# Kernel tuning notes

Hardware: AMD Instinct MI355X
Metric: run time of the kernel (lower is better)

Reference implementation:

```python
import jax, jax.numpy as jnp
import numpy as np

B, C, H, W = 4, 256, 64, 64
C4 = C // 4
EPS = 1e-5  # BatchNorm eps (torch default)


def setup_inputs() -> dict:
    key = jax.random.key(0)
    ks = jax.random.split(key, 24)
    rn = lambda k, s, sc=1.0: jax.random.normal(k, s, jnp.float32) * sc
    un = lambda k, s: jax.random.uniform(k, s, jnp.float32, 0.5, 1.5)
    return {
        "x1": rn(ks[0], (B, C, H, W)),
        "x2": rn(ks[1], (B, C, H, W)),
        "x3": rn(ks[2], (B, C, H, W)),
        # conv_n1: in_c -> in_c//4, 1x1 conv + BN(affine) params
        "w1": rn(ks[3], (C4, C), 0.05), "b1": rn(ks[4], (C4,), 0.05),
        "g1": 1.0 + rn(ks[5], (C4,), 0.05), "be1": rn(ks[6], (C4,), 0.05),
        "m1": rn(ks[7], (C4,), 0.05), "v1": un(ks[8], (C4,)),
        # conv_n2: in_c -> in_c//4
        "w2": rn(ks[9], (C4, C), 0.05), "b2": rn(ks[10], (C4,), 0.05),
        "g2": 1.0 + rn(ks[11], (C4,), 0.05), "be2": rn(ks[12], (C4,), 0.05),
        "m2": rn(ks[13], (C4,), 0.05), "v2": un(ks[14], (C4,)),
        # conv_n3: in_c -> in_c
        "w3": rn(ks[15], (C, C), 0.05), "b3": rn(ks[16], (C,), 0.05),
        "g3": 1.0 + rn(ks[17], (C,), 0.05), "be3": rn(ks[18], (C,), 0.05),
        "m3": rn(ks[19], (C,), 0.05), "v3": un(ks[20], (C,)),
        # gamma residual gate (torch inits to 0; use 0.5 so the attention path matters)
        "gam": jnp.full((1,), 0.5, jnp.float32),
    }


def _cbr(x, w, b, g, be, m, v):
    # 1x1 conv == channel contraction, then inference-mode BN, then ReLU
    y = jnp.einsum("bchw,oc->bohw", x, w) + b[None, :, None, None]
    scale = (g * jax.lax.rsqrt(v + EPS))[None, :, None, None]
    shift = (be - g * m * jax.lax.rsqrt(v + EPS))[None, :, None, None]
    return jax.nn.relu(y * scale + shift)


def reference(x1, x2, x3,
              w1, b1, g1, be1, m1, v1,
              w2, b2, g2, be2, m2, v2,
              w3, b3, g3, be3, m3, v3,
              gam):
    b, c, h, w = x1.shape
    hw = h * w
    q = _cbr(x1, w1, b1, g1, be1, m1, v1).reshape(b, -1, hw).transpose(0, 2, 1)  # (b, hw, c/4)
    k = _cbr(x2, w2, b2, g2, be2, m2, v2).reshape(b, -1, hw)                      # (b, c/4, hw)
    attn = jax.nn.softmax(jnp.einsum("bnc,bcm->bnm", q, k), axis=-1)              # (b, hw, hw)
    val = _cbr(x3, w3, b3, g3, be3, m3, v3).reshape(b, c, hw)                     # (b, c, hw)
    # out[b,c,i] = sum_j val[b,c,j] * attn[b,i,j]   (bmm with attn^T)
    out = jnp.einsum("bcj,bij->bci", val, attn).reshape(b, c, h, w)
    return gam[0] * out + x1
```

## Files before the change

kernel.cpp:

```cpp
#include <hip/hip_runtime.h>
#include <math.h>

#define HW 4096
#define CIN 256
#define BN_EPS 1e-5f
#define LOG2E 1.44269504088896f

typedef __attribute__((ext_vector_type(8))) short short8;
typedef __attribute__((ext_vector_type(4))) float floatx4;
typedef __attribute__((ext_vector_type(4))) unsigned short u16x4;
typedef unsigned short ushort;
typedef unsigned int u32;

__device__ inline ushort f2bf(float f) {
    union { float f; unsigned u; } c; c.f = f;
    unsigned r = c.u + 0x7fff + ((c.u >> 16) & 1);
    return (ushort)(r >> 16);
}
__device__ inline float bf2f(ushort u) {
    union { unsigned u; float f; } c; c.u = ((u32)u) << 16; return c.f;
}

__device__ inline void load_lds16(const ushort* g, ushort* l) {
    __builtin_amdgcn_global_load_lds(
        (const __attribute__((address_space(1))) u32*)g,
        (__attribute__((address_space(3))) u32*)l, 16, 0, 0);
}

__global__ __launch_bounds__(256) void transpose_bf16(
    const float* __restrict__ x1, const float* __restrict__ x2,
    const float* __restrict__ x3, ushort* __restrict__ Xt1,
    ushort* __restrict__ Xt2, ushort* __restrict__ Xt3)
{
    const int z = blockIdx.z;
    const int inp = z >> 2, b = z & 3;
    const float* x = inp == 0 ? x1 : (inp == 1 ? x2 : x3);
    ushort* o = inp == 0 ? Xt1 : (inp == 1 ? Xt2 : Xt3);
    const int c0 = blockIdx.y << 6, p0 = blockIdx.x << 6;
    const int tid = threadIdx.x;

    __shared__ float t[64 * 65];

    const int col = tid & 63, r4 = tid >> 6;
#pragma unroll
    for (int t2 = 0; t2 < 16; t2++) {
        int row = (t2 << 2) + r4;
        t[row * 65 + col] = x[((size_t)(b * CIN + c0 + row) << 12) + p0 + col];
    }
    __syncthreads();
    const int p = tid >> 2, cs = (tid & 3) << 4;
    alignas(16) ushort v[16];
#pragma unroll
    for (int k = 0; k < 16; k++) v[k] = f2bf(t[(cs + k) * 65 + p]);
    size_t base = ((size_t)(b * HW + p0 + p)) * 256 + c0 + cs;
    *(short8*)&o[base]     = *(short8*)&v[0];
    *(short8*)&o[base + 8] = *(short8*)&v[8];
}

__global__ __launch_bounds__(256) void prep_weights(
    const float* __restrict__ w1, const float* __restrict__ b1,
    const float* __restrict__ g1, const float* __restrict__ be1,
    const float* __restrict__ m1, const float* __restrict__ v1,
    const float* __restrict__ w2, const float* __restrict__ b2,
    const float* __restrict__ g2, const float* __restrict__ be2,
    const float* __restrict__ m2, const float* __restrict__ v2,
    const float* __restrict__ w3, const float* __restrict__ b3,
    const float* __restrict__ g3, const float* __restrict__ be3,
    const float* __restrict__ m3, const float* __restrict__ v3,
    ushort* __restrict__ w1c, ushort* __restrict__ w2c, ushort* __restrict__ w3c,
    float* __restrict__ bc)
{
    const int bid = blockIdx.x, tid = threadIdx.x;
    if (bid < 384) {
        int idx = bid * 256 + tid;
        if (idx < 16384) {
            int o = idx >> 8;
            float A = g1[o] * rsqrtf(v1[o] + BN_EPS) * LOG2E;
            w1c[idx] = f2bf(w1[idx] * A);
        } else if (idx < 32768) {
            int i2 = idx - 16384, o = i2 >> 8;
            float A = g2[o] * rsqrtf(v2[o] + BN_EPS);
            w2c[i2] = f2bf(w2[i2] * A);
        } else {
            int i3 = idx - 32768, o = i3 >> 8;
            float A = g3[o] * rsqrtf(v3[o] + BN_EPS);
            w3c[i3] = f2bf(w3[i3] * A);
        }
    } else {
        if (tid < 64) {
            float A = g1[tid] * rsqrtf(v1[tid] + BN_EPS);
            bc[tid] = ((b1[tid] - m1[tid]) * A + be1[tid]) * LOG2E;
        } else if (tid < 128) {
            int o = tid - 64;
            float A = g2[o] * rsqrtf(v2[o] + BN_EPS);
            bc[tid] = (b2[o] - m2[o]) * A + be2[o];
        } else {
#pragma unroll
            for (int t = 0; t < 2; t++) {
                int o = (tid - 128) + t * 128;
                float A = g3[o] * rsqrtf(v3[o] + BN_EPS);
                bc[128 + o] = (b3[o] - m3[o]) * A + be3[o];
            }
        }
    }
}

__global__ __launch_bounds__(256) void gemm_qk(
    const ushort* __restrict__ Xt1, const ushort* __restrict__ Xt2,
    const ushort* __restrict__ w1c, const ushort* __restrict__ w2c,
    const float* __restrict__ bc, ushort* __restrict__ Qw, ushort* __restrict__ Kw)
{
    const int which = blockIdx.z;
    const ushort* X = which ? Xt2 : Xt1;
    const ushort* W = which ? w2c : w1c;
    const float* bias = bc + which * 64;
    ushort* out = which ? Kw : Qw;
    const int b = blockIdx.y;
    const int px0 = blockIdx.x << 6;

    __shared__ alignas(16) ushort Wl[64 * 64];
    __shared__ alignas(16) ushort Xl[64 * 64];

    const int tid = threadIdx.x;
    const int lane = tid & 63;
    const int wv = tid >> 6;
    const int l15 = lane & 15, qd = lane >> 4;
    const int n0w = wv << 4;
    const int sw = l15 & 7;

    floatx4 acc[4];
#pragma unroll
    for (int mt = 0; mt < 4; mt++) acc[mt] = (floatx4){0.f, 0.f, 0.f, 0.f};

    for (int kk = 0; kk < 4; kk++) {
        const int k0 = kk << 6;
        __syncthreads();
#pragma unroll
        for (int t = 0; t < 2; t++) {
            int L = t * 256 + tid;
            int row = L >> 3, c = L & 7;
            load_lds16(W + row * 256 + k0 + ((c ^ (row & 7)) << 3), Wl + L * 8);
            load_lds16(X + ((size_t)(b * HW + px0 + row)) * 256 + k0 + ((c ^ (row & 7)) << 3),
                       Xl + L * 8);
        }
        __syncthreads();
#pragma unroll
        for (int kb = 0; kb < 2; kb++) {
            const int csel = (((kb << 2) + qd) ^ sw) << 3;
            short8 bfr = *(const short8*)&Xl[((n0w + l15) << 6) + csel];
#pragma unroll
            for (int mt = 0; mt < 4; mt++) {
                short8 af = *(const short8*)&Wl[(((mt << 4) + l15) << 6) + csel];
                acc[mt] = __builtin_amdgcn_mfma_f32_16x16x32_bf16(af, bfr, acc[mt], 0, 0, 0);
            }
        }
    }
    const int px = px0 + n0w + l15;
#pragma unroll
    for (int mt = 0; mt < 4; mt++) {
        alignas(8) ushort v4[4];
#pragma unroll
        for (int r = 0; r < 4; r++) {
            int oc = (mt << 4) + (qd << 2) + r;
            v4[r] = f2bf(fmaxf(acc[mt][r] + bias[oc], 0.f));
        }
        *(u16x4*)&out[(((size_t)(b * HW + px)) << 6) + (mt << 4) + (qd << 2)] = *(u16x4*)v4;
    }
}

__global__ __launch_bounds__(256) void gemm_v(
    const ushort* __restrict__ Xt3, const ushort* __restrict__ w3c,
    const float* __restrict__ bc, ushort* __restrict__ Vw)
{
    const int b = blockIdx.y;
    const int px0 = blockIdx.x << 6;
    const int oc0 = blockIdx.z << 7;
    const float* bias = bc + 128;

    __shared__ alignas(16) ushort Xl[64 * 64];
    __shared__ alignas(16) ushort Wl[128 * 64];

    const int tid = threadIdx.x;
    const int lane = tid & 63;
    const int wv = tid >> 6;
    const int l15 = lane & 15, qd = lane >> 4;
    const int wm0 = (wv & 1) << 5, wn0 = (wv >> 1) << 6;
    const int sw = l15 & 7;

    floatx4 acc[2][4];
#pragma unroll
    for (int mt = 0; mt < 2; mt++)
#pragma unroll
        for (int nt = 0; nt < 4; nt++) acc[mt][nt] = (floatx4){0.f, 0.f, 0.f, 0.f};

    for (int kk = 0; kk < 4; kk++) {
        const int k0 = kk << 6;
        __syncthreads();
#pragma unroll
        for (int t = 0; t < 2; t++) {
            int L = t * 256 + tid;
            int row = L >> 3, c = L & 7;
            load_lds16(Xt3 + ((size_t)(b * HW + px0 + row)) * 256 + k0 + ((c ^ (row & 7)) << 3),
                       Xl + L * 8);
        }
#pragma unroll
        for (int t = 0; t < 4; t++) {
            int L = t * 256 + tid;
            int row = L >> 3, c = L & 7;
            load_lds16(w3c + (oc0 + row) * 256 + k0 + ((c ^ (row & 7)) << 3), Wl + L * 8);
        }
        __syncthreads();
#pragma unroll
        for (int kb = 0; kb < 2; kb++) {
            const int csel = (((kb << 2) + qd) ^ sw) << 3;
            short8 af[2], bfr[4];
#pragma unroll
            for (int mt = 0; mt < 2; mt++)
                af[mt] = *(const short8*)&Xl[((wm0 + (mt << 4) + l15) << 6) + csel];
#pragma unroll
            for (int nt = 0; nt < 4; nt++)
                bfr[nt] = *(const short8*)&Wl[((wn0 + (nt << 4) + l15) << 6) + csel];
#pragma unroll
            for (int mt = 0; mt < 2; mt++)
#pragma unroll
                for (int nt = 0; nt < 4; nt++)
                    acc[mt][nt] = __builtin_amdgcn_mfma_f32_16x16x32_bf16(
                        af[mt], bfr[nt], acc[mt][nt], 0, 0, 0);
        }
    }
#pragma unroll
    for (int nt = 0; nt < 4; nt++) {
        int oc = oc0 + wn0 + (nt << 4) + l15;
        float bv = bias[oc];
#pragma unroll
        for (int mt = 0; mt < 2; mt++) {
            alignas(8) ushort v4[4];
#pragma unroll
            for (int r = 0; r < 4; r++)
                v4[r] = f2bf(fmaxf(acc[mt][nt][r] + bv, 0.f));
            size_t base = (((size_t)(b * CIN + oc)) << 12) + px0 + wm0 + (mt << 4) + (qd << 2);
            *(u16x4*)&Vw[base] = *(u16x4*)v4;
        }
    }
}

__global__ __launch_bounds__(512, 4) void flash_mfma(
    const ushort* __restrict__ Q, const ushort* __restrict__ K,
    const ushort* __restrict__ Vtg, ushort* __restrict__ Op0,
    ushort* __restrict__ Op1, float* __restrict__ mlM, float* __restrict__ mlL)
{
    const int tid = threadIdx.x;
    const int lane = tid & 63;
    const int wv = tid >> 6;
    const int it = wv & 3, ch = wv >> 2;
    const int l15 = lane & 15, qd = lane >> 4;
    const int sw = l15 & 7;

    const int bid = blockIdx.x;
    const int s = bid >> 8;
    const int r8 = bid & 255;
    const int b = (r8 & 7) >> 1;
    const int itile = ((r8 >> 3) << 1) | (r8 & 1);
    const int i0 = itile << 6;
    const int jbeg = s << 11;

    __shared__ alignas(16) ushort Kt[64 * 64];
    __shared__ alignas(16) ushort Vt[256 * 64];
    __shared__ alignas(16) ushort Pt[64 * 64];

    const int prow = it * 16 + l15;

    short8 qf[2];
#pragma unroll
    for (int kb = 0; kb < 2; kb++)
        qf[kb] = *(const short8*)(Q + (((size_t)((b << 12) + i0 + prow)) << 6) + kb * 32 + qd * 8);

    const floatx4 zv = {0.f, 0.f, 0.f, 0.f};
    floatx4 acc[8];
#pragma unroll
    for (int ct = 0; ct < 8; ct++) acc[ct] = zv;
    float mrun = -3.0e38f, lrun = 0.f;

    for (int jj = 0; jj < 2048; jj += 64) {
        const int j0 = jbeg + jj;
        __syncthreads();
        {
            int row = tid >> 3, cb = tid & 7;
            load_lds16(K + (((size_t)((b << 12) + j0 + row)) << 6) + ((cb ^ (row & 7)) << 3),
                       Kt + tid * 8);
#pragma unroll
            for (int t2 = 0; t2 < 4; t2++) {
                int idx = tid + (t2 << 9);
                int vr = idx >> 3, vc = idx & 7;
                load_lds16(Vtg + (((size_t)(b * CIN + vr)) << 12) + j0 + ((vc ^ (vr & 7)) << 3),
                           Vt + idx * 8);
            }
        }
        __syncthreads();

        floatx4 st[4];
#pragma unroll
        for (int t = 0; t < 4; t++) st[t] = zv;
#pragma unroll
        for (int kb = 0; kb < 2; kb++) {
            const int csel = (((kb << 2) + qd) ^ sw) << 3;
#pragma unroll
            for (int t = 0; t < 4; t++) {
                short8 kf = *(const short8*)&Kt[(((t << 4) + l15) << 6) + csel];
                st[t] = __builtin_amdgcn_mfma_f32_16x16x32_bf16(kf, qf[kb], st[t], 0, 0, 0);
            }
        }

        float mloc = -3.0e38f;
#pragma unroll
        for (int t = 0; t < 4; t++)
#pragma unroll
            for (int r = 0; r < 4; r++) mloc = fmaxf(mloc, st[t][r]);
        mloc = fmaxf(mloc, __shfl_xor(mloc, 16));
        mloc = fmaxf(mloc, __shfl_xor(mloc, 32));
        float mnew = fmaxf(mrun, mloc);

        float rs = 0.f;
#pragma unroll
        for (int t = 0; t < 4; t++)
#pragma unroll
            for (int r = 0; r < 4; r++) {
                float p = exp2f(st[t][r] - mnew);
                st[t][r] = p;
                rs += p;
            }
        rs += __shfl_xor(rs, 16);
        rs += __shfl_xor(rs, 32);
        float alpha = exp2f(mrun - mnew);
        mrun = mnew;
        lrun = lrun * alpha + rs;

        if (ch == 0) {
#pragma unroll
            for (int t = 0; t < 4; t++) {
                u16x4 pk;
#pragma unroll
                for (int r = 0; r < 4; r++) pk[r] = f2bf(st[t][r]);
                int jb8 = (t << 1) + (qd >> 1);
                *(u16x4*)&Pt[(prow << 6) + (((jb8 ^ sw) << 3) + ((qd & 1) << 2))] = pk;
            }
        }
        __syncthreads();

        if (__any(alpha < 1.0f)) {
#pragma unroll
            for (int ct = 0; ct < 8; ct++) acc[ct] *= alpha;
        }

        short8 pf[2];
#pragma unroll
        for (int kb = 0; kb < 2; kb++)
            pf[kb] = *(const short8*)&Pt[(prow << 6) + ((((kb << 2) + qd) ^ sw) << 3)];
#pragma unroll
        for (int kb = 0; kb < 2; kb++) {
            const int csel = (((kb << 2) + qd) ^ sw) << 3;
#pragma unroll
            for (int ct = 0; ct < 8; ct++) {
                int crow = (ch << 7) + (ct << 4) + l15;
                short8 vf = *(const short8*)&Vt[(crow << 6) + csel];
                acc[ct] = __builtin_amdgcn_mfma_f32_16x16x32_bf16(vf, pf[kb], acc[ct], 0, 0, 0);
            }
        }
    }

    ushort* Op = s ? Op1 : Op0;
    size_t obase = ((size_t)((b << 12) + i0 + prow)) << 8;
#pragma unroll
    for (int ct = 0; ct < 8; ct++) {
        u16x4 pk;
#pragma unroll
        for (int r = 0; r < 4; r++) pk[r] = f2bf(acc[ct][r]);
        *(u16x4*)&Op[obase + (ch << 7) + (ct << 4) + (qd << 2)] = pk;
    }
    if (ch == 0 && qd == 0) {
        int mi = (s << 14) + (b << 12) + i0 + prow;
        mlM[mi] = mrun;
        mlL[mi] = lrun;
    }
}

__global__ __launch_bounds__(256) void merge_out(
    const ushort* __restrict__ Op0, const ushort* __restrict__ Op1,
    const float* __restrict__ mlM, const float* __restrict__ mlL,
    const float* __restrict__ x1, const float* __restrict__ gam,
    float* __restrict__ out)
{
    const int b = blockIdx.z, c0 = blockIdx.y << 6, i0 = blockIdx.x << 6;
    const int tid = threadIdx.x;

    __shared__ float Tl[64][65];
    __shared__ float a0s[64], a1s[64];

    if (tid < 64) {
        int gi = (b << 12) + i0 + tid;
        float m0 = mlM[gi], m1 = mlM[16384 + gi];
        float l0 = mlL[gi], l1 = mlL[16384 + gi];
        float M = fmaxf(m0, m1);
        float w0 = exp2f(m0 - M), w1 = exp2f(m1 - M);
        float gd = gam[0] / (w0 * l0 + w1 * l1);
        a0s[tid] = w0 * gd;
        a1s[tid] = w1 * gd;
    }
    __syncthreads();
#pragma unroll
    for (int k = 0; k < 4; k++) {
        int idx4 = tid + (k << 8);
        int i = idx4 >> 4, c4 = (idx4 & 15) << 2;
        size_t g = ((size_t)((b << 12) + i0 + i)) * 256 + c0 + c4;
        u16x4 p0 = *(const u16x4*)&Op0[g];
        u16x4 p1 = *(const u16x4*)&Op1[g];
        float A0 = a0s[i], A1 = a1s[i];
#pragma unroll
        for (int r = 0; r < 4; r++)
            Tl[c4 + r][i] = A0 * bf2f(p0[r]) + A1 * bf2f(p1[r]);
    }
    __syncthreads();
#pragma unroll
    for (int k = 0; k < 4; k++) {
        int idx4 = tid + (k << 8);
        int c = idx4 >> 4, i4 = (idx4 & 15) << 2;
        size_t g = (((size_t)(b * CIN + c0 + c)) << 12) + i0 + i4;
        float4 xv = *(const float4*)&x1[g];
        float4 o;
        o.x = Tl[c][i4 + 0] + xv.x;
        o.y = Tl[c][i4 + 1] + xv.y;
        o.z = Tl[c][i4 + 2] + xv.z;
        o.w = Tl[c][i4 + 3] + xv.w;
        *(float4*)&out[g] = o;
    }
}

extern "C" void kernel_launch(void* const* d_in, const int* in_sizes, int n_in,
                              void* d_out, int out_size, void* d_ws, size_t ws_size,
                              hipStream_t stream)
{
    const float* x1  = (const float*)d_in[0];
    const float* x2  = (const float*)d_in[1];
    const float* x3  = (const float*)d_in[2];
    const float* w1  = (const float*)d_in[3];
    const float* b1  = (const float*)d_in[4];
    const float* g1  = (const float*)d_in[5];
    const float* be1 = (const float*)d_in[6];
    const float* m1  = (const float*)d_in[7];
    const float* v1  = (const float*)d_in[8];
    const float* w2  = (const float*)d_in[9];
    const float* b2  = (const float*)d_in[10];
    const float* g2  = (const float*)d_in[11];
    const float* be2 = (const float*)d_in[12];
    const float* m2  = (const float*)d_in[13];
    const float* v2  = (const float*)d_in[14];
    const float* w3  = (const float*)d_in[15];
    const float* b3  = (const float*)d_in[16];
    const float* g3  = (const float*)d_in[17];
    const float* be3 = (const float*)d_in[18];
    const float* m3  = (const float*)d_in[19];
    const float* v3  = (const float*)d_in[20];
    const float* gam = (const float*)d_in[21];

    ushort* Xt1 = (ushort*)d_ws;
    ushort* Xt2 = Xt1 + (size_t)4194304;
    ushort* Xt3 = Xt2 + (size_t)4194304;
    ushort* Qw  = Xt3 + (size_t)4194304;
    ushort* Kw  = Qw  + (size_t)1048576;
    ushort* Vw  = Kw  + (size_t)1048576;
    ushort* w1c = Vw  + (size_t)4194304;
    ushort* w2c = w1c + 16384;
    ushort* w3c = w2c + 16384;
    float*  bc  = (float*)(w3c + 65536);

    ushort* Op0 = Xt1;
    ushort* Op1 = Xt2;
    float*  mlM = (float*)Xt3;
    float*  mlL = mlM + 32768;

    transpose_bf16<<<dim3(64, 4, 12), 256, 0, stream>>>(x1, x2, x3, Xt1, Xt2, Xt3);
    prep_weights<<<385, 256, 0, stream>>>(w1, b1, g1, be1, m1, v1,
                                          w2, b2, g2, be2, m2, v2,
                                          w3, b3, g3, be3, m3, v3,
                                          w1c, w2c, w3c, bc);
    gemm_qk<<<dim3(64, 4, 2), 256, 0, stream>>>(Xt1, Xt2, w1c, w2c, bc, Qw, Kw);
    gemm_v <<<dim3(64, 4, 2), 256, 0, stream>>>(Xt3, w3c, bc, Vw);
    flash_mfma<<<512, 512, 0, stream>>>(Qw, Kw, Vw, Op0, Op1, mlM, mlL);
    merge_out<<<dim3(64, 4, 4), 256, 0, stream>>>(Op0, Op1, mlM, mlL, x1, gam, (float*)d_out);
}
```

Baseline: 240.2 us.

## Use Cauchy-Schwarz softmax bound, fuse prep kernels, and retile flash attention

Replaces the online softmax running max with a fixed per-row upper bound, ||q_i||·max_j||k_j||, computed in the QK GEMM epilogue through an atomicMax. This removes the per-tile max reductions and accumulator rescaling. The transpose and weight prep are fused into one launch, as are the Q/K and V GEMMs, and flash attention moves to 1024-thread blocks covering 128 query rows with K/V staging overlapped with compute. The fixed bound risks underflow of exp2 when the bound is loose, and the larger blocks reduce the number of workgroups.

```diff
diff --git a/kernel.cpp b/kernel.cpp
--- a/kernel.cpp
+++ b/kernel.cpp
@@ -27,37 +27,9 @@
         (__attribute__((address_space(3))) u32*)l, 16, 0, 0);
 }
 
-__global__ __launch_bounds__(256) void transpose_bf16(
+__global__ __launch_bounds__(256) void fuse_tp(
     const float* __restrict__ x1, const float* __restrict__ x2,
-    const float* __restrict__ x3, ushort* __restrict__ Xt1,
-    ushort* __restrict__ Xt2, ushort* __restrict__ Xt3)
-{
-    const int z = blockIdx.z;
-    const int inp = z >> 2, b = z & 3;
-    const float* x = inp == 0 ? x1 : (inp == 1 ? x2 : x3);
-    ushort* o = inp == 0 ? Xt1 : (inp == 1 ? Xt2 : Xt3);
-    const int c0 = blockIdx.y << 6, p0 = blockIdx.x << 6;
-    const int tid = threadIdx.x;
-
-    __shared__ float t[64 * 65];
-
-    const int col = tid & 63, r4 = tid >> 6;
-#pragma unroll
-    for (int t2 = 0; t2 < 16; t2++) {
-        int row = (t2 << 2) + r4;
-        t[row * 65 + col] = x[((size_t)(b * CIN + c0 + row) << 12) + p0 + col];
-    }
-    __syncthreads();
-    const int p = tid >> 2, cs = (tid & 3) << 4;
-    alignas(16) ushort v[16];
-#pragma unroll
-    for (int k = 0; k < 16; k++) v[k] = f2bf(t[(cs + k) * 65 + p]);
-    size_t base = ((size_t)(b * HW + p0 + p)) * 256 + c0 + cs;
-    *(short8*)&o[base]     = *(short8*)&v[0];
-    *(short8*)&o[base + 8] = *(short8*)&v[8];
-}
-
-__global__ __launch_bounds__(256) void prep_weights(
+    const float* __restrict__ x3,
     const float* __restrict__ w1, const float* __restrict__ b1,
     const float* __restrict__ g1, const float* __restrict__ be1,
     const float* __restrict__ m1, const float* __restrict__ v1,
@@ -67,320 +39,349 @@
     const float* __restrict__ w3, const float* __restrict__ b3,
     const float* __restrict__ g3, const float* __restrict__ be3,
     const float* __restrict__ m3, const float* __restrict__ v3,
+    ushort* __restrict__ Xt1, ushort* __restrict__ Xt2, ushort* __restrict__ Xt3,
     ushort* __restrict__ w1c, ushort* __restrict__ w2c, ushort* __restrict__ w3c,
-    float* __restrict__ bc)
+    float* __restrict__ bc, unsigned* __restrict__ KmxU)
 {
-    const int bid = blockIdx.x, tid = threadIdx.x;
-    if (bid < 384) {
-        int idx = bid * 256 + tid;
-        if (idx < 16384) {
-            int o = idx >> 8;
-            float A = g1[o] * rsqrtf(v1[o] + BN_EPS) * LOG2E;
-            w1c[idx] = f2bf(w1[idx] * A);
-        } else if (idx < 32768) {
-            int i2 = idx - 16384, o = i2 >> 8;
+    const int z = blockIdx.z;
+    const int tid = threadIdx.x;
+
+    __shared__ float t[64 * 65];
+
+    if (z == 12) {
+        int pid = blockIdx.y * 64 + blockIdx.x;
+        int g0 = pid * 256 + tid;
+        for (int g = g0; g < 98304; g += 65536) {
+            if (g < 16384) {
+                int o = g >> 8;
+                float A = g1[o] * rsqrtf(v1[o] + BN_EPS) * LOG2E;
+                w1c[g] = f2bf(w1[g] * A);
+            } else if (g < 32768) {
+                int i2 = g - 16384, o = i2 >> 8;
+                float A = g2[o] * rsqrtf(v2[o] + BN_EPS);
+                w2c[i2] = f2bf(w2[i2] * A);
+            } else {
+                int i3 = g - 32768, o = i3 >> 8;
+                float A = g3[o] * rsqrtf(v3[o] + BN_EPS);
+                w3c[i3] = f2bf(w3[i3] * A);
+            }
+        }
+        if (g0 < 4) KmxU[g0] = 0u;
+        if (g0 < 64) {
+            float A = g1[g0] * rsqrtf(v1[g0] + BN_EPS);
+            bc[g0] = ((b1[g0] - m1[g0]) * A + be1[g0]) * LOG2E;
+        } else if (g0 < 128) {
+            int o = g0 - 64;
             float A = g2[o] * rsqrtf(v2[o] + BN_EPS);
-            w2c[i2] = f2bf(w2[i2] * A);
-        } else {
-            int i3 = idx - 32768, o = i3 >> 8;
+            bc[g0] = (b2[o] - m2[o]) * A + be2[o];
+        } else if (g0 < 384) {
+            int o = g0 - 128;
             float A = g3[o] * rsqrtf(v3[o] + BN_EPS);
-            w3c[i3] = f2bf(w3[i3] * A);
-        }
-    } else {
-        if (tid < 64) {
-            float A = g1[tid] * rsqrtf(v1[tid] + BN_EPS);
-            bc[tid] = ((b1[tid] - m1[tid]) * A + be1[tid]) * LOG2E;
-        } else if (tid < 128) {
-            int o = tid - 64;
-            float A = g2[o] * rsqrtf(v2[o] + BN_EPS);
-            bc[tid] = (b2[o] - m2[o]) * A + be2[o];
-        } else {
-#pragma unroll
-            for (int t = 0; t < 2; t++) {
-                int o = (tid - 128) + t * 128;
-                float A = g3[o] * rsqrtf(v3[o] + BN_EPS);
-                bc[128 + o] = (b3[o] - m3[o]) * A + be3[o];
-            }
-        }
-    }
-}
-
-__global__ __launch_bounds__(256) void gemm_qk(
+            bc[128 + o] = (b3[o] - m3[o]) * A + be3[o];
+        }
+        return;
+    }
+
+    const int inp = z >> 2, b = z & 3;
+    const float* x = inp == 0 ? x1 : (inp == 1 ? x2 : x3);
+    ushort* o = inp == 0 ? Xt1 : (inp == 1 ? Xt2 : Xt3);
+    const int c0 = blockIdx.y << 6, p0 = blockIdx.x << 6;
+
+    const int col = tid & 63, r4 = tid >> 6;
+#pragma unroll
+    for (int t2 = 0; t2 < 16; t2++) {
+        int row = (t2 << 2) + r4;
+        t[row * 65 + col] = x[((size_t)(b * CIN + c0 + row) << 12) + p0 + col];
+    }
+    __syncthreads();
+    const int p = tid >> 2, cs = (tid & 3) << 4;
+    alignas(16) ushort v[16];
+#pragma unroll
+    for (int k = 0; k < 16; k++) v[k] = f2bf(t[(cs + k) * 65 + p]);
+    size_t base = ((size_t)(b * HW + p0 + p)) * 256 + c0 + cs;
+    *(short8*)&o[base]     = *(short8*)&v[0];
+    *(short8*)&o[base + 8] = *(short8*)&v[8];
+}
+
+__global__ __launch_bounds__(256) void gemm_qkv(
     const ushort* __restrict__ Xt1, const ushort* __restrict__ Xt2,
+    const ushort* __restrict__ Xt3,
     const ushort* __restrict__ w1c, const ushort* __restrict__ w2c,
-    const float* __restrict__ bc, ushort* __restrict__ Qw, ushort* __restrict__ Kw)
+    const ushort* __restrict__ w3c, const float* __restrict__ bc,
+    ushort* __restrict__ Qw, ushort* __restrict__ Kw, ushort* __restrict__ Vw,
+    float* __restrict__ Qn, unsigned* __restrict__ KmxU)
 {
-    const int which = blockIdx.z;
-    const ushort* X = which ? Xt2 : Xt1;
-    const ushort* W = which ? w2c : w1c;
-    const float* bias = bc + which * 64;
-    ushort* out = which ? Kw : Qw;
+    const int z = blockIdx.z;
     const int b = blockIdx.y;
     const int px0 = blockIdx.x << 6;
-
-    __shared__ alignas(16) ushort Wl[64 * 64];
-    __shared__ alignas(16) ushort Xl[64 * 64];
-
-    const int tid = threadIdx.x;
-    const int lane = tid & 63;
-    const int wv = tid >> 6;
+    const int tid = threadIdx.x, lane = tid & 63, wv = tid >> 6;
     const int l15 = lane & 15, qd = lane >> 4;
-    const int n0w = wv << 4;
     const int sw = l15 & 7;
-
-    floatx4 acc[4];
-#pragma unroll
-    for (int mt = 0; mt < 4; mt++) acc[mt] = (floatx4){0.f, 0.f, 0.f, 0.f};
-
-    for (int kk = 0; kk < 4; kk++) {
-        const int k0 = kk << 6;
-        __syncthreads();
-#pragma unroll
-        for (int t = 0; t < 2; t++) {
-            int L = t * 256 + tid;
-            int row = L >> 3, c = L & 7;
-            load_lds16(W + row * 256 + k0 + ((c ^ (row & 7)) << 3), Wl + L * 8);
-            load_lds16(X + ((size_t)(b * HW + px0 + row)) * 256 + k0 + ((c ^ (row & 7)) << 3),
-                       Xl + L * 8);
-        }
-        __syncthreads();
-#pragma unroll
-        for (int kb = 0; kb < 2; kb++) {
-            const int csel = (((kb << 2) + qd) ^ sw) << 3;
-            short8 bfr = *(const short8*)&Xl[((n0w + l15) << 6) + csel];
-#pragma unroll
-            for (int mt = 0; mt < 4; mt++) {
-                short8 af = *(const short8*)&Wl[(((mt << 4) + l15) << 6) + csel];
-                acc[mt] = __builtin_amdgcn_mfma_f32_16x16x32_bf16(af, bfr, acc[mt], 0, 0, 0);
-            }
-        }
-    }
-    const int px = px0 + n0w + l15;
-#pragma unroll
-    for (int mt = 0; mt < 4; mt++) {
-        alignas(8) ushort v4[4];
-#pragma unroll
-        for (int r = 0; r < 4; r++) {
-            int oc = (mt << 4) + (qd << 2) + r;
-            v4[r] = f2bf(fmaxf(acc[mt][r] + bias[oc], 0.f));
-        }
-        *(u16x4*)&out[(((size_t)(b * HW + px)) << 6) + (mt << 4) + (qd << 2)] = *(u16x4*)v4;
-    }
-}
-
-__global__ __launch_bounds__(256) void gemm_v(
-    const ushort* __restrict__ Xt3, const ushort* __restrict__ w3c,
-    const float* __restrict__ bc, ushort* __restrict__ Vw)
-{
-    const int b = blockIdx.y;
-    const int px0 = blockIdx.x << 6;
-    const int oc0 = blockIdx.z << 7;
-    const float* bias = bc + 128;
 
     __shared__ alignas(16) ushort Xl[64 * 64];
     __shared__ alignas(16) ushort Wl[128 * 64];
 
-    const int tid = threadIdx.x;
-    const int lane = tid & 63;
-    const int wv = tid >> 6;
-    const int l15 = lane & 15, qd = lane >> 4;
-    const int wm0 = (wv & 1) << 5, wn0 = (wv >> 1) << 6;
-    const int sw = l15 & 7;
-
-    floatx4 acc[2][4];
-#pragma unroll
-    for (int mt = 0; mt < 2; mt++)
-#pragma unroll
-        for (int nt = 0; nt < 4; nt++) acc[mt][nt] = (floatx4){0.f, 0.f, 0.f, 0.f};
-
-    for (int kk = 0; kk < 4; kk++) {
-        const int k0 = kk << 6;
-        __syncthreads();
-#pragma unroll
-        for (int t = 0; t < 2; t++) {
-            int L = t * 256 + tid;
-            int row = L >> 3, c = L & 7;
-            load_lds16(Xt3 + ((size_t)(b * HW + px0 + row)) * 256 + k0 + ((c ^ (row & 7)) << 3),
-                       Xl + L * 8);
-        }
-#pragma unroll
-        for (int t = 0; t < 4; t++) {
-            int L = t * 256 + tid;
-            int row = L >> 3, c = L & 7;
-            load_lds16(w3c + (oc0 + row) * 256 + k0 + ((c ^ (row & 7)) << 3), Wl + L * 8);
-        }
-        __syncthreads();
-#pragma unroll
-        for (int kb = 0; kb < 2; kb++) {
-            const int csel = (((kb << 2) + qd) ^ sw) << 3;
-            short8 af[2], bfr[4];
-#pragma unroll
-            for (int mt = 0; mt < 2; mt++)
-                af[mt] = *(const short8*)&Xl[((wm0 + (mt << 4) + l15) << 6) + csel];
-#pragma unroll
-            for (int nt = 0; nt < 4; nt++)
-                bfr[nt] = *(const short8*)&Wl[((wn0 + (nt << 4) + l15) << 6) + csel];
-#pragma unroll
-            for (int mt = 0; mt < 2; mt++)
+    if (z < 2) {
+        const ushort* X = z ? Xt2 : Xt1;
+        const ushort* W = z ? w2c : w1c;
+        const float* bias = bc + (z << 6);
+        ushort* out = z ? Kw : Qw;
+        const int n0w = wv << 4;
+
+        floatx4 acc[4];
+#pragma unroll
+        for (int mt = 0; mt < 4; mt++) acc[mt] = (floatx4){0.f, 0.f, 0.f, 0.f};
+
+        for (int kk = 0; kk < 4; kk++) {
+            const int k0 = kk << 6;
+            __syncthreads();
+#pragma unroll
+            for (int t = 0; t < 2; t++) {
+                int L = t * 256 + tid;
+                int row = L >> 3, c8 = L & 7;
+                load_lds16(W + row * 256 + k0 + ((c8 ^ (row & 7)) << 3), Wl + L * 8);
+                load_lds16(X + ((size_t)((b << 12) + px0 + row)) * 256 + k0 +
+                               ((c8 ^ (row & 7)) << 3), Xl + L * 8);
+            }
+            __syncthreads();
+#pragma unroll
+            for (int kb = 0; kb < 2; kb++) {
+                const int csel = (((kb << 2) + qd) ^ sw) << 3;
+                short8 bfr = *(const short8*)&Xl[((n0w + l15) << 6) + csel];
+#pragma unroll
+                for (int mt = 0; mt < 4; mt++) {
+                    short8 af = *(const short8*)&Wl[(((mt << 4) + l15) << 6) + csel];
+                    acc[mt] = __builtin_amdgcn_mfma_f32_16x16x32_bf16(af, bfr, acc[mt], 0, 0, 0);
+                }
+            }
+        }
+        const int px = px0 + n0w + l15;
+        float s2 = 0.f;
+#pragma unroll
+        for (int mt = 0; mt < 4; mt++) {
+            alignas(8) ushort v4[4];
+#pragma unroll
+            for (int r = 0; r < 4; r++) {
+                int oc = (mt << 4) + (qd << 2) + r;
+                float y = fmaxf(acc[mt][r] + bias[oc], 0.f);
+                s2 += y * y;
+                v4[r] = f2bf(y);
+            }
+            *(u16x4*)&out[(((size_t)((b << 12) + px)) << 6) + (mt << 4) + (qd << 2)] =
+                *(u16x4*)v4;
+        }
+        s2 += __shfl_xor(s2, 16);
+        s2 += __shfl_xor(s2, 32);
+        if (z == 0) {
+            if (qd == 0) Qn[(b << 12) + px] = sqrtf(s2);
+        } else {
+#pragma unroll
+            for (int off = 1; off < 16; off <<= 1) s2 = fmaxf(s2, __shfl_xor(s2, off));
+            if (lane == 0) atomicMax(KmxU + b, __float_as_uint(sqrtf(s2)));
+        }
+    } else {
+        const int oc0 = (z - 2) << 7;
+        const float* bias = bc + 128;
+        const int wm0 = (wv & 1) << 5, wn0 = (wv >> 1) << 6;
+
+        floatx4 acc[2][4];
+#pragma unroll
+        for (int mt = 0; mt < 2; mt++)
+#pragma unroll
+            for (int nt = 0; nt < 4; nt++) acc[mt][nt] = (floatx4){0.f, 0.f, 0.f, 0.f};
+
+        for (int kk = 0; kk < 4; kk++) {
+            const int k0 = kk << 6;
+            __syncthreads();
+#pragma unroll
+            for (int t = 0; t < 2; t++) {
+                int L = t * 256 + tid;
+                int row = L >> 3, c8 = L & 7;
+                load_lds16(Xt3 + ((size_t)((b << 12) + px0 + row)) * 256 + k0 +
+                               ((c8 ^ (row & 7)) << 3), Xl + L * 8);
+            }
+#pragma unroll
+            for (int t = 0; t < 4; t++) {
+                int L = t * 256 + tid;
+                int row = L >> 3, c8 = L & 7;
+                load_lds16(w3c + (oc0 + row) * 256 + k0 + ((c8 ^ (row & 7)) << 3), Wl + L * 8);
+            }
+            __syncthreads();
+#pragma unroll
+            for (int kb = 0; kb < 2; kb++) {
+                const int csel = (((kb << 2) + qd) ^ sw) << 3;
+                short8 af[2], bfr[4];
+#pragma unroll
+                for (int mt = 0; mt < 2; mt++)
+                    af[mt] = *(const short8*)&Xl[((wm0 + (mt << 4) + l15) << 6) + csel];
 #pragma unroll
                 for (int nt = 0; nt < 4; nt++)
-                    acc[mt][nt] = __builtin_amdgcn_mfma_f32_16x16x32_bf16(
-                        af[mt], bfr[nt], acc[mt][nt], 0, 0, 0);
-        }
-    }
-#pragma unroll
-    for (int nt = 0; nt < 4; nt++) {
-        int oc = oc0 + wn0 + (nt << 4) + l15;
-        float bv = bias[oc];
-#pragma unroll
-        for (int mt = 0; mt < 2; mt++) {
-            alignas(8) ushort v4[4];
-#pragma unroll
-            for (int r = 0; r < 4; r++)
-                v4[r] = f2bf(fmaxf(acc[mt][nt][r] + bv, 0.f));
-            size_t base = (((size_t)(b * CIN + oc)) << 12) + px0 + wm0 + (mt << 4) + (qd << 2);
-            *(u16x4*)&Vw[base] = *(u16x4*)v4;
-        }
-    }
-}
-
-__global__ __launch_bounds__(512, 4) void flash_mfma(
+                    bfr[nt] = *(const short8*)&Wl[((wn0 + (nt << 4) + l15) << 6) + csel];
+#pragma unroll
+                for (int mt = 0; mt < 2; mt++)
+#pragma unroll
+                    for (int nt = 0; nt < 4; nt++)
+                        acc[mt][nt] = __builtin_amdgcn_mfma_f32_16x16x32_bf16(
+                            af[mt], bfr[nt], acc[mt][nt], 0, 0, 0);
+            }
+        }
+#pragma unroll
+        for (int nt = 0; nt < 4; nt++) {
+            int oc = oc0 + wn0 + (nt << 4) + l15;
+            float bv = bias[oc];
+#pragma unroll
+            for (int mt = 0; mt < 2; mt++) {
+                alignas(8) ushort v4[4];
+#pragma unroll
+                for (int r = 0; r < 4; r++)
+                    v4[r] = f2bf(fmaxf(acc[mt][nt][r] + bv, 0.f));
+                size_t base = (((size_t)(b * CIN + oc)) << 12) + px0 + wm0 + (mt << 4) + (qd << 2);
+                *(u16x4*)&Vw[base] = *(u16x4*)v4;
+            }
+        }
+    }
+}
+
+__global__ __launch_bounds__(1024, 4) void flash_mfma(
     const ushort* __restrict__ Q, const ushort* __restrict__ K,
-    const ushort* __restrict__ Vtg, ushort* __restrict__ Op0,
+    const ushort* __restrict__ Vtg, const float* __restrict__ Qn,
+    const unsigned* __restrict__ KmxU, ushort* __restrict__ Op0,
     ushort* __restrict__ Op1, float* __restrict__ mlM, float* __restrict__ mlL)
 {
     const int tid = threadIdx.x;
     const int lane = tid & 63;
     const int wv = tid >> 6;
-    const int it = wv & 3, ch = wv >> 2;
     const int l15 = lane & 15, qd = lane >> 4;
     const int sw = l15 & 7;
+    const int jh = wv >> 3;
+    const int si = (wv & 7) << 4;
+    const int iw = wv & 1, ch = wv >> 1;
 
     const int bid = blockIdx.x;
-    const int s = bid >> 8;
-    const int r8 = bid & 255;
-    const int b = (r8 & 7) >> 1;
-    const int itile = ((r8 >> 3) << 1) | (r8 & 1);
-    const int i0 = itile << 6;
+    const int s = bid & 1;
+    const int b = (bid >> 1) & 3;
+    const int i0 = (bid >> 3) << 7;
     const int jbeg = s << 11;
 
     __shared__ alignas(16) ushort Kt[64 * 64];
     __shared__ alignas(16) ushort Vt[256 * 64];
-    __shared__ alignas(16) ushort Pt[64 * 64];
-
-    const int prow = it * 16 + l15;
+    __shared__ alignas(16) ushort Pt[128 * 64];
+    __shared__ float lred[2][128];
+
+    const float kmx = __uint_as_float(KmxU[b]);
+    const int iS = i0 + si + l15;
+    const float Mi = Qn[(b << 12) + iS] * kmx;
 
     short8 qf[2];
 #pragma unroll
     for (int kb = 0; kb < 2; kb++)
-        qf[kb] = *(const short8*)(Q + (((size_t)((b << 12) + i0 + prow)) << 6) + kb * 32 + qd * 8);
+        qf[kb] = *(const short8*)(Q + (((size_t)((b << 12) + iS)) << 6) + kb * 32 + qd * 8);
 
     const floatx4 zv = {0.f, 0.f, 0.f, 0.f};
-    floatx4 acc[8];
-#pragma unroll
-    for (int ct = 0; ct < 8; ct++) acc[ct] = zv;
-    float mrun = -3.0e38f, lrun = 0.f;
-
-    for (int jj = 0; jj < 2048; jj += 64) {
-        const int j0 = jbeg + jj;
-        __syncthreads();
-        {
-            int row = tid >> 3, cb = tid & 7;
-            load_lds16(K + (((size_t)((b << 12) + j0 + row)) << 6) + ((cb ^ (row & 7)) << 3),
-                       Kt + tid * 8);
-#pragma unroll
-            for (int t2 = 0; t2 < 4; t2++) {
-                int idx = tid + (t2 << 9);
-                int vr = idx >> 3, vc = idx & 7;
-                load_lds16(Vtg + (((size_t)(b * CIN + vr)) << 12) + j0 + ((vc ^ (vr & 7)) << 3),
-                           Vt + idx * 8);
-            }
-        }
-        __syncthreads();
-
-        floatx4 st[4];
-#pragma unroll
-        for (int t = 0; t < 4; t++) st[t] = zv;
+    floatx4 acc[2][4];
+#pragma unroll
+    for (int ct = 0; ct < 2; ct++)
+#pragma unroll
+        for (int is = 0; is < 4; is++) acc[ct][is] = zv;
+    float lsum = 0.f;
+
+#define STAGE_K(J0)                                                              \
+    if (tid < 512) {                                                             \
+        int row = tid >> 3, c8 = tid & 7;                                        \
+        load_lds16(K + (((size_t)((b << 12) + (J0) + row)) << 6) +               \
+                       ((c8 ^ (row & 7)) << 3), Kt + tid * 8);                   \
+    }
+#define STAGE_V(J0)                                                              \
+    {                                                                            \
+        _Pragma("unroll")                                                        \
+        for (int t2 = 0; t2 < 2; t2++) {                                         \
+            int idx = tid + (t2 << 10);                                          \
+            int vr = idx >> 3, vc = idx & 7;                                     \
+            load_lds16(Vtg + (((size_t)((b << 8) + vr)) << 12) + (J0) +          \
+                           ((vc ^ (vr & 7)) << 3), Vt + idx * 8);                \
+        }                                                                        \
+    }
+
+    STAGE_K(jbeg)
+    STAGE_V(jbeg)
+    __syncthreads();
+
+    for (int jj = 0; jj < 32; jj++) {
+        const int j0n = jbeg + ((jj + 1) << 6);
+
+        floatx4 st[2] = {zv, zv};
 #pragma unroll
         for (int kb = 0; kb < 2; kb++) {
             const int csel = (((kb << 2) + qd) ^ sw) << 3;
 #pragma unroll
-            for (int t = 0; t < 4; t++) {
-                short8 kf = *(const short8*)&Kt[(((t << 4) + l15) << 6) + csel];
-                st[t] = __builtin_amdgcn_mfma_f32_16x16x32_bf16(kf, qf[kb], st[t], 0, 0, 0);
-            }
-        }
-
-        float mloc = -3.0e38f;
-#pragma unroll
-        for (int t = 0; t < 4; t++)
-#pragma unroll
-            for (int r = 0; r < 4; r++) mloc = fmaxf(mloc, st[t][r]);
-        mloc = fmaxf(mloc, __shfl_xor(mloc, 16));
-        mloc = fmaxf(mloc, __shfl_xor(mloc, 32));
-        float mnew = fmaxf(mrun, mloc);
-
-        float rs = 0.f;
-#pragma unroll
-        for (int t = 0; t < 4; t++)
-#pragma unroll
-            for (int r = 0; r < 4; r++) {
-                float p = exp2f(st[t][r] - mnew);
-                st[t][r] = p;
-                rs += p;
-            }
-        rs += __shfl_xor(rs, 16);
-        rs += __shfl_xor(rs, 32);
-        float alpha = exp2f(mrun - mnew);
-        mrun = mnew;
-        lrun = lrun * alpha + rs;
-
-        if (ch == 0) {
-#pragma unroll
-            for (int t = 0; t < 4; t++) {
-                u16x4 pk;
-#pragma unroll
-                for (int r = 0; r < 4; r++) pk[r] = f2bf(st[t][r]);
-                int jb8 = (t << 1) + (qd >> 1);
-                *(u16x4*)&Pt[(prow << 6) + (((jb8 ^ sw) << 3) + ((qd & 1) << 2))] = pk;
-            }
+            for (int jt = 0; jt < 2; jt++) {
+                short8 kf = *(const short8*)&Kt[(((jh << 5) + (jt << 4) + l15) << 6) + csel];
+                st[jt] = __builtin_amdgcn_mfma_f32_16x16x32_bf16(kf, qf[kb], st[jt], 0, 0, 0);
+            }
+        }
+
+        const int prow = si + l15;
+#pragma unroll
+        for (int jt = 0; jt < 2; jt++) {
+            float p0 = exp2f(st[jt][0] - Mi);
+            float p1 = exp2f(st[jt][1] - Mi);
+            float p2 = exp2f(st[jt][2] - Mi);
+            float p3 = exp2f(st[jt][3] - Mi);
+            lsum += (p0 + p1) + (p2 + p3);
+            alignas(8) ushort pk[4] = {f2bf(p0), f2bf(p1), f2bf(p2), f2bf(p3)};
+            int c8 = (jh << 2) + (jt << 1) + (qd >> 1);
+            *(u16x4*)&Pt[(prow << 6) + ((c8 ^ sw) << 3) + ((qd & 1) << 2)] = *(u16x4*)pk;
         }
         __syncthreads();
 
-        if (__any(alpha < 1.0f)) {
-#pragma unroll
-            for (int ct = 0; ct < 8; ct++) acc[ct] *= alpha;
-        }
-
-        short8 pf[2];
-#pragma unroll
-        for (int kb = 0; kb < 2; kb++)
-            pf[kb] = *(const short8*)&Pt[(prow << 6) + ((((kb << 2) + qd) ^ sw) << 3)];
+        if (jj + 1 < 32) STAGE_K(j0n)
+
 #pragma unroll
         for (int kb = 0; kb < 2; kb++) {
             const int csel = (((kb << 2) + qd) ^ sw) << 3;
-#pragma unroll
-            for (int ct = 0; ct < 8; ct++) {
-                int crow = (ch << 7) + (ct << 4) + l15;
-                short8 vf = *(const short8*)&Vt[(crow << 6) + csel];
-                acc[ct] = __builtin_amdgcn_mfma_f32_16x16x32_bf16(vf, pf[kb], acc[ct], 0, 0, 0);
-            }
-        }
-    }
+            short8 vf[2], pf[4];
+#pragma unroll
+            for (int ct = 0; ct < 2; ct++)
+                vf[ct] = *(const short8*)&Vt[(((ch << 5) + (ct << 4) + l15) << 6) + csel];
+#pragma unroll
+            for (int is = 0; is < 4; is++)
+                pf[is] = *(const short8*)&Pt[(((iw << 6) + (is << 4) + l15) << 6) + csel];
+#pragma unroll
+            for (int ct = 0; ct < 2; ct++)
+#pragma unroll
+                for (int is = 0; is < 4; is++)
+                    acc[ct][is] = __builtin_amdgcn_mfma_f32_16x16x32_bf16(
+                        vf[ct], pf[is], acc[ct][is], 0, 0, 0);
+        }
+        __syncthreads();
+
+        if (jj + 1 < 32) STAGE_V(j0n)
+    }
+#undef STAGE_K
+#undef STAGE_V
+
+    lsum += __shfl_xor(lsum, 16);
+    lsum += __shfl_xor(lsum, 32);
+    if (qd == 0) lred[jh][si + l15] = lsum;
+    __syncthreads();
 
     ushort* Op = s ? Op1 : Op0;
-    size_t obase = ((size_t)((b << 12) + i0 + prow)) << 8;
-#pragma unroll
-    for (int ct = 0; ct < 8; ct++) {
-        u16x4 pk;
-#pragma unroll
-        for (int r = 0; r < 4; r++) pk[r] = f2bf(acc[ct][r]);
-        *(u16x4*)&Op[obase + (ch << 7) + (ct << 4) + (qd << 2)] = pk;
-    }
-    if (ch == 0 && qd == 0) {
-        int mi = (s << 14) + (b << 12) + i0 + prow;
-        mlM[mi] = mrun;
-        mlL[mi] = lrun;
+#pragma unroll
+    for (int is = 0; is < 4; is++) {
+        int i = i0 + (iw << 6) + (is << 4) + l15;
+        size_t obase = (((size_t)((b << 12) + i)) << 8);
+#pragma unroll
+        for (int ct = 0; ct < 2; ct++) {
+            alignas(8) ushort pk[4];
+#pragma unroll
+            for (int r = 0; r < 4; r++) pk[r] = f2bf(acc[ct][is][r]);
+            *(u16x4*)&Op[obase + (ch << 5) + (ct << 4) + (qd << 2)] = *(u16x4*)pk;
+        }
+    }
+    if (jh == 0 && qd == 0) {
+        int mi2 = (s << 14) + (b << 12) + iS;
+        mlM[mi2] = Mi;
+        mlL[mi2] = lred[0][si + l15] + lred[1][si + l15];
     }
 }
 
@@ -472,19 +473,22 @@
     ushort* w2c = w1c + 16384;
     ushort* w3c = w2c + 16384;
     float*  bc  = (float*)(w3c + 65536);
+    float*  Qn  = bc + 384;
+    unsigned* KmxU = (unsigned*)(Qn + 16384);
 
     ushort* Op0 = Xt1;
     ushort* Op1 = Xt2;
     float*  mlM = (float*)Xt3;
     float*  mlL = mlM + 32768;
 
-    transpose_bf16<<<dim3(64, 4, 12), 256, 0, stream>>>(x1, x2, x3, Xt1, Xt2, Xt3);
-    prep_weights<<<385, 256, 0, stream>>>(w1, b1, g1, be1, m1, v1,
-                                          w2, b2, g2, be2, m2, v2,
-                                          w3, b3, g3, be3, m3, v3,
-                                          w1c, w2c, w3c, bc);
-    gemm_qk<<<dim3(64, 4, 2), 256, 0, stream>>>(Xt1, Xt2, w1c, w2c, bc, Qw, Kw);
-    gemm_v <<<dim3(64, 4, 2), 256, 0, stream>>>(Xt3, w3c, bc, Vw);
-    flash_mfma<<<512, 512, 0, stream>>>(Qw, Kw, Vw, Op0, Op1, mlM, mlL);
+    fuse_tp<<<dim3(64, 4, 13), 256, 0, stream>>>(
+        x1, x2, x3,
+        w1, b1, g1, be1, m1, v1,
+        w2, b2, g2, be2, m2, v2,
+        w3, b3, g3, be3, m3, v3,
+        Xt1, Xt2, Xt3, w1c, w2c, w3c, bc, KmxU);
+    gemm_qkv<<<dim3(64, 4, 4), 256, 0, stream>>>(
+        Xt1, Xt2, Xt3, w1c, w2c, w3c, bc, Qw, Kw, Vw, Qn, KmxU);
+    flash_mfma<<<256, 1024, 0, stream>>>(Qw, Kw, Vw, Qn, KmxU, Op0, Op1, mlM, mlL);
     merge_out<<<dim3(64, 4, 4), 256, 0, stream>>>(Op0, Op1, mlM, mlL, x1, gam, (float*)d_out);
 }
```

Result: faster. 213.7 us (-11.0%).
